# Performance work log

Hardware: AMD Instinct MI355X
Metric: run time of the kernel (lower is better)

## Reference

```python
import jax, jax.numpy as jnp
import numpy as np

HEADS, FOLD_W, FOLD_H, PW, PH = 4, 2, 2, 2, 2


def setup_inputs() -> dict:
    key = jax.random.key(0)
    ks = jax.random.split(key, 4)
    B, C, W0, H0 = 64, 128, 56, 56
    hd = HEADS * 24  # 96
    return {
        "x": jax.random.normal(ks[0], (B, C, W0, H0), jnp.float32),
        "Wc": jax.random.normal(ks[1], (hd, C), jnp.float32) * 0.05,
        "bc": jnp.zeros((hd,), jnp.float32),
        "Wp": jax.random.normal(ks[2], (hd, C), jnp.float32) * 0.05,
        "bp": jnp.zeros((hd,), jnp.float32),
        "sim_alpha": jnp.ones((1,), jnp.float32),
        "sim_beta": jnp.zeros((1,), jnp.float32),
        "Wo": jax.random.normal(ks[3], (C, hd), jnp.float32) * 0.05,
        "bo": jnp.zeros((C,), jnp.float32),
    }


def _conv1x1(t, W, b):
    return jnp.einsum('oc,bcwh->bowh', W, t) + b[None, :, None, None]


def _forward(x, Wc, bc, Wp, bp, sim_alpha, sim_beta, Wo, bo):
    B, C, W0, H0 = x.shape
    value = _conv1x1(x, Wp, bp)   # [B, e*c, W0, H0]
    q = _conv1x1(x, Wc, bc)
    hd = q.shape[1] // HEADS
    # 'b (e c) w h -> (b e) c w h'
    split = lambda t: t.reshape(B * HEADS, hd, W0, H0)
    value, q = split(value), split(q)
    # fold: 'b c (f1 w) (f2 h) -> (b f1 f2) c w h'
    w2, h2 = W0 // FOLD_W, H0 // FOLD_H
    def fold(t):
        b0 = t.shape[0]
        return (t.reshape(b0, hd, FOLD_W, w2, FOLD_H, h2)
                 .transpose(0, 2, 4, 1, 3, 5)
                 .reshape(b0 * FOLD_W * FOLD_H, hd, w2, h2))
    value, q = fold(value), fold(q)
    b, c, w, h = q.shape
    # adaptive avg pool to (PW, PH): mean over equal blocks
    def adpool(t):
        return t.reshape(b, c, PW, w // PW, PH, h // PH).mean(axis=(3, 5))
    centers = adpool(q).reshape(b, c, PW * PH).transpose(0, 2, 1)          # [b, M, c]
    value_centers = adpool(value).reshape(b, c, PW * PH).transpose(0, 2, 1)
    qf = q.reshape(b, c, w * h).transpose(0, 2, 1)                          # [b, N, c]
    vf = value.reshape(b, c, w * h).transpose(0, 2, 1)
    eps = 1e-12
    cn = centers / jnp.clip(jnp.linalg.norm(centers, axis=-1, keepdims=True), eps)
    xn = qf / jnp.clip(jnp.linalg.norm(qf, axis=-1, keepdims=True), eps)
    sim = jax.nn.sigmoid(sim_beta + sim_alpha * jnp.einsum('bmc,bnc->bmn', cn, xn))  # [b, M, N]
    # hard top-1 assignment over centers axis
    idx = jnp.argmax(sim, axis=1)                                           # [b, N]
    mask = (jnp.arange(sim.shape[1])[None, :, None] == idx[:, None, :])
    sim = sim * mask
    # weighted combine (segment-sum over patches) instead of huge broadcast
    cluster = (jnp.einsum('bmn,bnc->bmc', sim, vf) + value_centers) / (sim.sum(-1, keepdims=True) + 1.0)
    patches = jnp.einsum('bmn,bmc->bnc', sim, cluster)                      # [b, N, c]
    patches = patches.transpose(0, 2, 1).reshape(b, c, w, h)
    # unfold: '(b f1 f2) c w h -> b c (f1 w) (f2 h)'
    patches = (patches.reshape(B * HEADS, FOLD_W, FOLD_H, c, w, h)
                      .transpose(0, 3, 1, 4, 2, 5)
                      .reshape(B * HEADS, c, W0, H0))
    patches = patches.reshape(B, HEADS * c, W0, H0)
    return _conv1x1(patches, Wo, bo)


def reference(x, Wc, bc, Wp, bp, sim_alpha, sim_beta, Wo, bo):
    return _forward(x, Wc, bc, Wp, bp, sim_alpha, sim_beta, Wo, bo)
```

## Files before the change

kernel.cpp:

```cpp
#include <hip/hip_runtime.h>
#include <math.h>

#define CIN 128
#define HD  96
#define SP  3136
#define ROW 56
#define SLAB 1568
#define YSTRIDE 9216

__global__ __launch_bounds__(256) void pe_k(
    const float* __restrict__ Wo, const float* __restrict__ Wp,
    const float* __restrict__ bp, float* __restrict__ P, float* __restrict__ obp)
{
  const int e = blockIdx.x;
  __shared__ float ws[24][128];
  const int tid = threadIdx.x;
  for (int i = tid; i < 24 * 128; i += 256)
    ws[i >> 7][i & 127] = Wp[(size_t)(e * 24 + (i >> 7)) * CIN + (i & 127)];
  __syncthreads();
  const int co = tid & 127;
  const int cig = tid >> 7;
  float wo_r[24];
  #pragma unroll
  for (int c = 0; c < 24; ++c) wo_r[c] = Wo[(size_t)co * HD + e * 24 + c];
  for (int ci = cig * 64; ci < cig * 64 + 64; ++ci) {
    float s = 0.f;
    #pragma unroll
    for (int c = 0; c < 24; ++c) s = fmaf(wo_r[c], ws[c][ci], s);
    P[((size_t)e * 128 + ci) * 128 + co] = s;
  }
  if (cig == 0) {
    float s = 0.f;
    #pragma unroll
    for (int c = 0; c < 24; ++c) s = fmaf(wo_r[c], bp[e * 24 + c], s);
    obp[e * 128 + co] = s;
  }
}

__global__ __launch_bounds__(128) void q_conv(
    const float* __restrict__ x, const float* __restrict__ Wc,
    const float* __restrict__ bc, float* __restrict__ qbuf)
{
  const int st = blockIdx.x % 49;
  const int b  = blockIdx.x / 49;
  const float* xb = x + (size_t)b * CIN * SP + st * 64;

  __shared__ float xs[32][64];
  __shared__ float wl[32][100];

  const int tid = threadIdx.x;
  const int og = tid >> 4;
  const int sg = tid & 15;

  float acc[12][4];
  #pragma unroll
  for (int i = 0; i < 12; ++i) { acc[i][0]=0.f; acc[i][1]=0.f; acc[i][2]=0.f; acc[i][3]=0.f; }

  for (int kt = 0; kt < 4; ++kt) {
    __syncthreads();
    #pragma unroll
    for (int r = 0; r < 4; ++r) {
      int i = tid + r * 128;
      int cc = i >> 4, s4 = i & 15;
      float4 v = *reinterpret_cast<const float4*>(xb + (size_t)(kt*32 + cc) * SP + s4*4);
      *reinterpret_cast<float4*>(&xs[cc][s4*4]) = v;
    }
    #pragma unroll
    for (int r = 0; r < 6; ++r) {
      int i = tid + r * 128;
      int o  = i >> 3, c4 = i & 7;
      float4 wv = *reinterpret_cast<const float4*>(Wc + (size_t)o * CIN + kt*32 + c4*4);
      wl[c4*4+0][o] = wv.x; wl[c4*4+1][o] = wv.y;
      wl[c4*4+2][o] = wv.z; wl[c4*4+3][o] = wv.w;
    }
    __syncthreads();
    #pragma unroll
    for (int cc = 0; cc < 32; ++cc) {
      float xv[4];
      *reinterpret_cast<float4*>(xv) = *reinterpret_cast<const float4*>(&xs[cc][sg*4]);
      float wv[12];
      *reinterpret_cast<float4*>(wv + 0) = *reinterpret_cast<const float4*>(&wl[cc][og*12 + 0]);
      *reinterpret_cast<float4*>(wv + 4) = *reinterpret_cast<const float4*>(&wl[cc][og*12 + 4]);
      *reinterpret_cast<float4*>(wv + 8) = *reinterpret_cast<const float4*>(&wl[cc][og*12 + 8]);
      #pragma unroll
      for (int i = 0; i < 12; ++i)
        #pragma unroll
        for (int j = 0; j < 4; ++j)
          acc[i][j] = fmaf(wv[i], xv[j], acc[i][j]);
    }
  }
  #pragma unroll
  for (int i = 0; i < 12; ++i) {
    const int o = og * 12 + i;
    const float bias = bc[o];
    float4 v;
    v.x = acc[i][0] + bias; v.y = acc[i][1] + bias;
    v.z = acc[i][2] + bias; v.w = acc[i][3] + bias;
    *reinterpret_cast<float4*>(qbuf + ((size_t)b*96 + o) * SP + st*64 + sg*4) = v;
  }
}

__global__ __launch_bounds__(512, 4) void cluster_k(
    float* qbuf, const float* __restrict__ alpha_p, const float* __restrict__ beta_p)
{
  const int blk = blockIdx.x;
  const int f1  = blk & 1;
  const int be  = blk >> 1;
  const size_t base = (size_t)be * 24 * SP + (size_t)(f1 * 28) * ROW;
  float* qp = qbuf + base;

  __shared__ double cnd[24][8];
  __shared__ float  sbest[SLAB];
  __shared__ unsigned char ibest[SLAB];
  __shared__ float dnl[8];

  const int tid  = threadIdx.x;
  const int wid  = tid >> 6;
  const int lane = tid & 63;

  for (int c = wid; c < 24; c += 8) {
    const float* src = qp + (size_t)c * SP;
    double b0=0,b1=0,b2=0,b3=0,b4=0,b5=0,b6=0,b7=0;
    for (int n = lane; n < SLAB; n += 64) {
      const int w = n / 56, h = n - w * 56;
      const int hf = (h >= 28) ? (h - 28) : h;
      const int g  = ((h >= 28) ? 4 : 0) + ((w >= 14) ? 2 : 0) + ((hf >= 14) ? 1 : 0);
      const double val = (double)src[n];
      b0 += (g==0)?val:0.0; b1 += (g==1)?val:0.0;
      b2 += (g==2)?val:0.0; b3 += (g==3)?val:0.0;
      b4 += (g==4)?val:0.0; b5 += (g==5)?val:0.0;
      b6 += (g==6)?val:0.0; b7 += (g==7)?val:0.0;
    }
    #pragma unroll
    for (int m = 32; m >= 1; m >>= 1) {
      b0 += __shfl_xor(b0,m); b1 += __shfl_xor(b1,m);
      b2 += __shfl_xor(b2,m); b3 += __shfl_xor(b3,m);
      b4 += __shfl_xor(b4,m); b5 += __shfl_xor(b5,m);
      b6 += __shfl_xor(b6,m); b7 += __shfl_xor(b7,m);
    }
    if (lane == 0) {
      cnd[c][0]=b0*(1.0/196.0); cnd[c][1]=b1*(1.0/196.0);
      cnd[c][2]=b2*(1.0/196.0); cnd[c][3]=b3*(1.0/196.0);
      cnd[c][4]=b4*(1.0/196.0); cnd[c][5]=b5*(1.0/196.0);
      cnd[c][6]=b6*(1.0/196.0); cnd[c][7]=b7*(1.0/196.0);
    }
  }
  __syncthreads();
  if (tid < 8) {
    double s = 0.0;
    #pragma unroll
    for (int c = 0; c < 24; ++c) { double t = cnd[c][tid]; s += t * t; }
    const double inv = 1.0 / fmax(sqrt(s), 1e-12);
    #pragma unroll
    for (int c = 0; c < 24; ++c) cnd[c][tid] *= inv;
  }
  __syncthreads();

  const double alpha = (double)alpha_p[0];
  const double beta  = (double)beta_p[0];

  for (int n0 = tid; n0 < SLAB; n0 += 512) {
    const int h  = n0 % 56;
    const int gb = (h >= 28) ? 4 : 0;
    double z0=0,z1=0,z2=0,z3=0,nrm=0;
    for (int c = 0; c < 24; ++c) {
      const double qv = (double)qp[(size_t)c * SP + n0];
      z0 += cnd[c][gb+0]*qv; z1 += cnd[c][gb+1]*qv;
      z2 += cnd[c][gb+2]*qv; z3 += cnd[c][gb+3]*qv;
      nrm += qv*qv;
    }
    const double inv = 1.0 / fmax(sqrt(nrm), 1e-12);
    const double v0 = beta + alpha * (z0 * inv);
    const double v1 = beta + alpha * (z1 * inv);
    const double v2 = beta + alpha * (z2 * inv);
    const double v3 = beta + alpha * (z3 * inv);
    double zb = v0; int bi = 0;
    if (v1 > zb) { zb = v1; bi = 1; }
    if (v2 > zb) { zb = v2; bi = 2; }
    if (v3 > zb) { zb = v3; bi = 3; }
    sbest[n0] = (float)(1.0 / (1.0 + exp(-zb)));
    ibest[n0] = (unsigned char)(gb + bi);
  }
  __syncthreads();

  if (wid < 8) {
    float dn = 0.f;
    for (int ch = 0; ch < 25; ++ch) {
      const int n = ch * 64 + lane;
      const bool p = (n < SLAB) && (ibest[n] == (unsigned char)wid);
      dn += p ? sbest[n] : 0.f;
    }
    #pragma unroll
    for (int m = 32; m >= 1; m >>= 1) dn += __shfl_xor(dn, m);
    if (lane == 0) dnl[wid] = dn;
  }
  __syncthreads();

  for (int i = tid; i < SLAB; i += 512) {
    qp[i] = sbest[i];
    reinterpret_cast<unsigned int*>(qp + SP)[i] = (unsigned int)ibest[i];
  }
  if (tid < 8) qp[2 * (size_t)SP + tid] = dnl[tid];
}

__global__ __launch_bounds__(256, 2) void seg_k(
    float* qbuf, const float* __restrict__ x)
{
  const int bid = blockIdx.x;
  const int wh  = bid & 1;
  const int f2  = (bid >> 1) & 1;
  const int f1  = (bid >> 2) & 1;
  const int b   = bid >> 3;

  __shared__ float4 sq_l[392];
  __shared__ unsigned int gq_l[392];
  __shared__ float xT[56][130];
  __shared__ float ysum[16][128];
  __shared__ float xps[2][128];

  const int tid = threadIdx.x;
  const int c   = tid & 127;
  const int pg  = tid >> 7;

  for (int n = tid; n < 392; n += 256) {
    const int r = n / 28, hc = n - r * 28;
    const int n_slab = (wh * 14 + r) * 56 + f2 * 28 + hc;
    float4 s4; unsigned int gp = 0;
    #pragma unroll
    for (int e = 0; e < 4; ++e) {
      const float* qp = qbuf + (size_t)(b*4 + e) * 24 * SP + (size_t)(f1*28) * ROW;
      const float sv = qp[n_slab];
      const unsigned int gv = reinterpret_cast<const unsigned int*>(qp + SP)[n_slab];
      if (e==0) s4.x = sv; else if (e==1) s4.y = sv;
      else if (e==2) s4.z = sv; else s4.w = sv;
      gp |= (gv & 3u) << (2*e);
    }
    sq_l[n] = s4; gq_l[n] = gp;
  }

  float sa[16];
  #pragma unroll
  for (int i = 0; i < 16; ++i) sa[i] = 0.f;
  float xp0 = 0.f, xp1 = 0.f;

  const float* xb = x + (size_t)b * CIN * SP;
  const int rowbase = f1*28 + wh*14;

  for (int ch = 0; ch < 7; ++ch) {
    __syncthreads();
    #pragma unroll
    for (int k = 0; k < 7; ++k) {
      const int slot = tid + k * 256;
      const int c2 = slot / 14, p4 = slot - c2 * 14;
      const int rr = p4 / 7, col4 = p4 - rr * 7;
      const int w = rowbase + ch*2 + rr;
      const float4 v = *reinterpret_cast<const float4*>(
          xb + (size_t)c2 * SP + (size_t)w * ROW + f2*28 + col4*4);
      const int pxl = rr * 28 + col4 * 4;
      xT[pxl+0][c2] = v.x; xT[pxl+1][c2] = v.y;
      xT[pxl+2][c2] = v.z; xT[pxl+3][c2] = v.w;
    }
    __syncthreads();
    for (int i = 0; i < 28; ++i) {
      const int pxl = 2*i + pg;
      const int n   = ch*56 + pxl;
      const float4 s4 = sq_l[n];
      const int gp = __builtin_amdgcn_readfirstlane((int)gq_l[n]);
      const float xv = xT[pxl][c];
      {
        const int k = gp & 3;
        if      (k == 0) sa[0]  += s4.x * xv;
        else if (k == 1) sa[1]  += s4.x * xv;
        else if (k == 2) sa[2]  += s4.x * xv;
        else             sa[3]  += s4.x * xv;
      }
      {
        const int k = (gp >> 2) & 3;
        if      (k == 0) sa[4]  += s4.y * xv;
        else if (k == 1) sa[5]  += s4.y * xv;
        else if (k == 2) sa[6]  += s4.y * xv;
        else             sa[7]  += s4.y * xv;
      }
      {
        const int k = (gp >> 4) & 3;
        if      (k == 0) sa[8]  += s4.z * xv;
        else if (k == 1) sa[9]  += s4.z * xv;
        else if (k == 2) sa[10] += s4.z * xv;
        else             sa[11] += s4.z * xv;
      }
      {
        const int k = (gp >> 6) & 3;
        if      (k == 0) sa[12] += s4.w * xv;
        else if (k == 1) sa[13] += s4.w * xv;
        else if (k == 2) sa[14] += s4.w * xv;
        else             sa[15] += s4.w * xv;
      }
      const int hc = (pxl >= 28) ? (pxl - 28) : pxl;
      if (hc >= 14) xp1 += xv; else xp0 += xv;
    }
  }

  __syncthreads();
  if (pg == 0) {
    #pragma unroll
    for (int k = 0; k < 16; ++k) ysum[k][c] = sa[k];
    xps[0][c] = xp0; xps[1][c] = xp1;
  }
  __syncthreads();
  if (pg == 1) {
    #pragma unroll
    for (int k = 0; k < 16; ++k) ysum[k][c] += sa[k];
    xps[0][c] += xp0; xps[1][c] += xp1;
  }
  __syncthreads();

  float* ybase = qbuf + ((size_t)b*96 + 9) * SP + (size_t)f1 * YSTRIDE;
  for (int i = tid; i < 16*128; i += 256) {
    const int row = i >> 7, cc = i & 127;
    ybase[((wh*2 + f2)*16 + row)*128 + cc] = ysum[row][cc];
  }
  {
    const int hb = tid >> 7, cc = tid & 127;
    ybase[64*128 + (f2*4 + wh*2 + hb)*128 + cc] = xps[hb][cc];
  }
}

__global__ __launch_bounds__(256) void proj_k(
    float* qbuf, const float* __restrict__ P, const float* __restrict__ obp)
{
  const int bid = blockIdx.x;
  const int b = bid >> 1, f1 = bid & 1;
  __shared__ float ylds[32][128];
  __shared__ float invs[32];
  const int tid = threadIdx.x;

  if (tid < 32) {
    const int e = tid >> 3, g = tid & 7;
    const float* dnp = qbuf + ((size_t)(b*4 + e) * 24 + 2) * SP + (size_t)(f1*28) * ROW;
    invs[tid] = 1.f / (dnp[g] + 1.f);
  }
  __syncthreads();

  const float* yp = qbuf + ((size_t)b*96 + 9) * SP + (size_t)f1 * YSTRIDE;
  for (int i = tid; i < 32*128; i += 256) {
    const int eg = i >> 7, cc = i & 127;
    const int e = eg >> 3, g = eg & 7, ff2 = g >> 2, m = g & 3;
    const float v = yp[((0 + ff2)*16 + e*4 + m)*128 + cc]
                  + yp[((2 + ff2)*16 + e*4 + m)*128 + cc]
                  + yp[64*128 + g*128 + cc] * (1.f/196.f);
    ylds[eg][cc] = v * invs[eg];
  }
  __syncthreads();

  const int co = tid & 127;
  const int e0 = (tid >> 7) * 2;
  float a0[8], a1[8];
  const float o0 = obp[e0 * 128 + co], o1 = obp[(e0 + 1) * 128 + co];
  #pragma unroll
  for (int g = 0; g < 8; ++g) { a0[g] = o0; a1[g] = o1; }
  for (int ci = 0; ci < 128; ++ci) {
    const float p0 = P[((size_t)e0 * 128 + ci) * 128 + co];
    const float p1 = P[((size_t)(e0 + 1) * 128 + ci) * 128 + co];
    #pragma unroll
    for (int g = 0; g < 8; ++g) {
      a0[g] = fmaf(p0, ylds[e0 * 8 + g][ci], a0[g]);
      a1[g] = fmaf(p1, ylds[(e0 + 1) * 8 + g][ci], a1[g]);
    }
  }
  float* pout = qbuf + ((size_t)b * 96 + 3 + f1 * 3) * SP;
  #pragma unroll
  for (int g = 0; g < 8; ++g) {
    pout[(e0 * 8 + g) * 128 + co]       = a0[g];
    pout[((e0 + 1) * 8 + g) * 128 + co] = a1[g];
  }
}

__global__ __launch_bounds__(256) void out_k(
    const float* __restrict__ qbuf, const float* __restrict__ bo,
    float* __restrict__ out)
{
  const int bid = blockIdx.x;
  const int b   = bid / 28;
  const int rem = bid % 28;
  const int f1  = rem / 14;
  const int rp  = rem % 14;
  const int n0  = rp * 112;

  __shared__ float  proj_l[4096];
  __shared__ float4 s_l4[112];
  __shared__ unsigned int g_l[112];
  __shared__ float  out_l[56 * 132];

  const int tid = threadIdx.x;

  {
    const float4* pg = reinterpret_cast<const float4*>(
        qbuf + ((size_t)b * 96 + 3 + f1*3) * SP);
    float4* pl = reinterpret_cast<float4*>(proj_l);
    #pragma unroll
    for (int r = 0; r < 4; ++r) pl[tid + r * 256] = pg[tid + r * 256];
  }
  for (int i = tid; i < 112; i += 256) {
    float4 sv; unsigned int gp = 0;
    #pragma unroll
    for (int e = 0; e < 4; ++e) {
      const float* sp = qbuf + ((size_t)(b*4 + e) * 24) * SP + (size_t)(f1*28) * ROW;
      const float sval = sp[n0 + i];
      const unsigned int gv = reinterpret_cast<const unsigned int*>(sp + SP)[n0 + i];
      if (e == 0) sv.x = sval; else if (e == 1) sv.y = sval;
      else if (e == 2) sv.z = sval; else sv.w = sval;
      gp |= (gv & 7u) << (8 * e);
    }
    s_l4[i] = sv; g_l[i] = gp;
  }
  __syncthreads();

  const int cq  = tid & 31;
  const int sub = tid >> 5;
  const float4 bo4 = *reinterpret_cast<const float4*>(bo + cq * 4);
  const float4* pl4 = reinterpret_cast<const float4*>(proj_l);

  for (int chunk = 0; chunk < 2; ++chunk) {
    const int pbase = chunk * 56;
    #pragma unroll
    for (int i = 0; i < 7; ++i) {
      const int pxl = sub * 7 + i;
      const int px  = pbase + pxl;
      const float4 sv = s_l4[px];
      const unsigned int gp = g_l[px];
      float4 acc = bo4;
      {
        const float4 p = pl4[(0*8 + (gp        & 7u)) * 32 + cq];
        acc.x = fmaf(sv.x, p.x, acc.x); acc.y = fmaf(sv.x, p.y, acc.y);
        acc.z = fmaf(sv.x, p.z, acc.z); acc.w = fmaf(sv.x, p.w, acc.w);
      }
      {
        const float4 p = pl4[(1*8 + ((gp >> 8) & 7u)) * 32 + cq];
        acc.x = fmaf(sv.y, p.x, acc.x); acc.y = fmaf(sv.y, p.y, acc.y);
        acc.z = fmaf(sv.y, p.z, acc.z); acc.w = fmaf(sv.y, p.w, acc.w);
      }
      {
        const float4 p = pl4[(2*8 + ((gp >> 16) & 7u)) * 32 + cq];
        acc.x = fmaf(sv.z, p.x, acc.x); acc.y = fmaf(sv.z, p.y, acc.y);
        acc.z = fmaf(sv.z, p.z, acc.z); acc.w = fmaf(sv.z, p.w, acc.w);
      }
      {
        const float4 p = pl4[(3*8 + ((gp >> 24) & 7u)) * 32 + cq];
        acc.x = fmaf(sv.w, p.x, acc.x); acc.y = fmaf(sv.w, p.y, acc.y);
        acc.z = fmaf(sv.w, p.z, acc.z); acc.w = fmaf(sv.w, p.w, acc.w);
      }
      *reinterpret_cast<float4*>(&out_l[pxl * 132 + cq * 4]) = acc;
    }
    __syncthreads();
    for (int t = tid; t < 128 * 56; t += 256) {
      const int co = t / 56, pxl = t - co * 56;
      out[((size_t)b * 128 + co) * SP + (size_t)f1 * SLAB + n0 + pbase + pxl] =
          out_l[pxl * 132 + co];
    }
    __syncthreads();
  }
}

extern "C" void kernel_launch(void* const* d_in, const int* in_sizes, int n_in,
                              void* d_out, int out_size, void* d_ws, size_t ws_size,
                              hipStream_t stream) {
  const float* x  = (const float*)d_in[0];
  const float* Wc = (const float*)d_in[1];
  const float* bc = (const float*)d_in[2];
  const float* Wp = (const float*)d_in[3];
  const float* bp = (const float*)d_in[4];
  const float* sa = (const float*)d_in[5];
  const float* sb = (const float*)d_in[6];
  const float* Wo = (const float*)d_in[7];
  const float* bo = (const float*)d_in[8];
  float* out  = (float*)d_out;
  float* qbuf = (float*)d_ws;
  float* Pbuf = out;
  float* obpb = out + 65536;

  pe_k     <<<dim3(4),       dim3(256), 0, stream>>>(Wo, Wp, bp, Pbuf, obpb);
  q_conv   <<<dim3(64 * 49), dim3(128), 0, stream>>>(x, Wc, bc, qbuf);
  cluster_k<<<dim3(512),     dim3(512), 0, stream>>>(qbuf, sa, sb);
  seg_k    <<<dim3(512),     dim3(256), 0, stream>>>(qbuf, x);
  proj_k   <<<dim3(128),     dim3(256), 0, stream>>>(qbuf, Pbuf, obpb);
  out_k    <<<dim3(1792),    dim3(256), 0, stream>>>(qbuf, bo, out);
}
```

Before: 230.1 us.

## Pre-transpose Wc and register-prefetch next K tile in q_conv

Adds a small kernel that transposes Wc into a [128][96] layout in scratch space inside the output buffer, so q_conv can store weights to shared memory with float4 writes instead of scalar transposed stores. q_conv also now loads the next K-tile of x and weights into registers while the current tile is being computed, overlapping global loads with the FMA loop. This costs an extra kernel launch and more registers per thread, and the shared-memory row padding is removed, which may introduce bank conflicts.

```diff
diff --git a/kernel.cpp b/kernel.cpp
--- a/kernel.cpp
+++ b/kernel.cpp
@@ -8,6 +8,15 @@
 #define SLAB 1568
 #define YSTRIDE 9216
 
+__global__ __launch_bounds__(256) void wtq_k(
+    const float* __restrict__ Wc, float* __restrict__ Wt)
+{
+  const int idx = blockIdx.x * 256 + threadIdx.x;
+  if (idx >= 96 * 128) return;
+  const int o = idx >> 7, c = idx & 127;
+  Wt[c * 96 + o] = Wc[idx];
+}
+
 __global__ __launch_bounds__(256) void pe_k(
     const float* __restrict__ Wo, const float* __restrict__ Wp,
     const float* __restrict__ bp, float* __restrict__ P, float* __restrict__ obp)
@@ -38,7 +47,7 @@
 }
 
 __global__ __launch_bounds__(128) void q_conv(
-    const float* __restrict__ x, const float* __restrict__ Wc,
+    const float* __restrict__ x, const float* __restrict__ Wt,
     const float* __restrict__ bc, float* __restrict__ qbuf)
 {
   const int st = blockIdx.x % 49;
@@ -46,7 +55,7 @@
   const float* xb = x + (size_t)b * CIN * SP + st * 64;
 
   __shared__ float xs[32][64];
-  __shared__ float wl[32][100];
+  __shared__ float wl[32][96];
 
   const int tid = threadIdx.x;
   const int og = tid >> 4;
@@ -56,24 +65,45 @@
   #pragma unroll
   for (int i = 0; i < 12; ++i) { acc[i][0]=0.f; acc[i][1]=0.f; acc[i][2]=0.f; acc[i][3]=0.f; }
 
+  float4 xr[4], wr[6];
+  #pragma unroll
+  for (int r = 0; r < 4; ++r) {
+    const int i = tid + r * 128;
+    xr[r] = *reinterpret_cast<const float4*>(xb + (size_t)(i >> 4) * SP + (i & 15) * 4);
+  }
+  #pragma unroll
+  for (int r = 0; r < 6; ++r) {
+    const int i = tid + r * 128;
+    wr[r] = *reinterpret_cast<const float4*>(Wt + (size_t)(i / 24) * 96 + (i % 24) * 4);
+  }
+
   for (int kt = 0; kt < 4; ++kt) {
     __syncthreads();
     #pragma unroll
     for (int r = 0; r < 4; ++r) {
-      int i = tid + r * 128;
-      int cc = i >> 4, s4 = i & 15;
-      float4 v = *reinterpret_cast<const float4*>(xb + (size_t)(kt*32 + cc) * SP + s4*4);
-      *reinterpret_cast<float4*>(&xs[cc][s4*4]) = v;
+      const int i = tid + r * 128;
+      *reinterpret_cast<float4*>(&xs[i >> 4][(i & 15) * 4]) = xr[r];
     }
     #pragma unroll
     for (int r = 0; r < 6; ++r) {
-      int i = tid + r * 128;
-      int o  = i >> 3, c4 = i & 7;
-      float4 wv = *reinterpret_cast<const float4*>(Wc + (size_t)o * CIN + kt*32 + c4*4);
-      wl[c4*4+0][o] = wv.x; wl[c4*4+1][o] = wv.y;
-      wl[c4*4+2][o] = wv.z; wl[c4*4+3][o] = wv.w;
+      const int i = tid + r * 128;
+      *reinterpret_cast<float4*>(&wl[i / 24][(i % 24) * 4]) = wr[r];
     }
     __syncthreads();
+    if (kt < 3) {
+      #pragma unroll
+      for (int r = 0; r < 4; ++r) {
+        const int i = tid + r * 128;
+        xr[r] = *reinterpret_cast<const float4*>(
+            xb + (size_t)((kt + 1) * 32 + (i >> 4)) * SP + (i & 15) * 4);
+      }
+      #pragma unroll
+      for (int r = 0; r < 6; ++r) {
+        const int i = tid + r * 128;
+        wr[r] = *reinterpret_cast<const float4*>(
+            Wt + (size_t)((kt + 1) * 32 + i / 24) * 96 + (i % 24) * 4);
+      }
+    }
     #pragma unroll
     for (int cc = 0; cc < 32; ++cc) {
       float xv[4];
@@ -477,9 +507,11 @@
   float* qbuf = (float*)d_ws;
   float* Pbuf = out;
   float* obpb = out + 65536;
-
+  float* Wtq  = out + 66048;
+
+  wtq_k    <<<dim3(48),      dim3(256), 0, stream>>>(Wc, Wtq);
   pe_k     <<<dim3(4),       dim3(256), 0, stream>>>(Wo, Wp, bp, Pbuf, obpb);
-  q_conv   <<<dim3(64 * 49), dim3(128), 0, stream>>>(x, Wc, bc, qbuf);
+  q_conv   <<<dim3(64 * 49), dim3(128), 0, stream>>>(x, Wtq, bc, qbuf);
   cluster_k<<<dim3(512),     dim3(512), 0, stream>>>(qbuf, sa, sb);
   seg_k    <<<dim3(512),     dim3(256), 0, stream>>>(qbuf, x);
   proj_k   <<<dim3(128),     dim3(256), 0, stream>>>(qbuf, Pbuf, obpb);
```

Result: slower. 294.2 us (+27.9%).
